# Kernel tuning notes

Hardware: AMD Instinct MI355X
Metric: run time of the kernel (lower is better)

The kernel has to match this reference:

```python
import jax, jax.numpy as jnp
import numpy as np

DIM = 2048
BATCH = 64


def setup_inputs() -> dict:
    key = jax.random.key(0)
    kx, kq, kk, kv = jax.random.split(key, 4)
    s = 1.0 / np.sqrt(DIM).astype(np.float32)  # keep q*k logits O(1)
    x = jax.random.normal(kx, (BATCH, DIM), dtype=jnp.float32)
    Wq = jax.random.normal(kq, (DIM, DIM), dtype=jnp.float32) * s
    Wk = jax.random.normal(kk, (DIM, DIM), dtype=jnp.float32) * s
    Wv = jax.random.normal(kv, (DIM, DIM), dtype=jnp.float32) * s
    return {"x": x, "Wq": Wq, "Wk": Wk, "Wv": Wv}


def reference(x, Wq, Wk, Wv):
    # nn.Linear(dim, inner_dim, bias=False): y = x @ W.T, W: [inner_dim, dim]
    q = x @ Wq.T  # [b, N]  (head_dim = 1, so each token's q is a scalar)
    k = x @ Wk.T  # [b, N]
    v = x @ Wv.T  # [b, N]
    # dot[b,i,j] = q[b,i] * k[b,j]  (rank-1 outer product per batch)
    logits = q[:, :, None] * k[:, None, :]  # [b, N, N]
    attn = jax.nn.softmax(logits, axis=-1)
    out = jnp.einsum("bij,bj->bi", attn, v)  # [b, N]
    # dim == inner_dim -> scale is Identity
    return out
```

## Files before the change

### kernel.cpp

```cpp
#include <hip/hip_runtime.h>
#include <hip/hip_bf16.h>

#define DIM 2048
#define NB  64
#define KSL 4
#define JSL 2

typedef short bf16x8 __attribute__((ext_vector_type(8)));
typedef short s16x4  __attribute__((ext_vector_type(4)));
typedef float f32x4  __attribute__((ext_vector_type(4)));
typedef float f32x2  __attribute__((ext_vector_type(2)));

__device__ __forceinline__ unsigned short f32_to_bf16_rne(float f) {
  unsigned u = __builtin_bit_cast(unsigned, f);
  unsigned r = u + 0x7FFF + ((u >> 16) & 1);
  return (unsigned short)(r >> 16);
}

__global__ __launch_bounds__(256)
void prep(const float* __restrict__ x, unsigned short* __restrict__ xrh,
          unsigned short* __restrict__ xrl, float* __restrict__ qkv) {
  const int tg = blockIdx.x * 256 + threadIdx.x;
#pragma unroll
  for (int z = 0; z < 3; ++z)
    *(float4*)(qkv + ((size_t)z * 32768 + tg) * 4) = make_float4(0.f,0.f,0.f,0.f);

  const int b = tg >> 9;
  const int k = (tg & 511) * 4;
  float4 f = *(const float4*)(x + (size_t)b * DIM + k);
  const int mt = b >> 4, l15 = b & 15;
  const int ck = k >> 5, quad = (k >> 3) & 3, u = k & 7;
  const size_t off = (((size_t)(mt * 64 + ck) * 64) + quad * 16 + l15) * 8 + u;
  float vf[4] = {f.x, f.y, f.z, f.w};
  ushort4 h4, l4;
  unsigned short* hp = &h4.x;
  unsigned short* lp = &l4.x;
#pragma unroll
  for (int e = 0; e < 4; ++e) {
    unsigned short h = f32_to_bf16_rne(vf[e]);
    float hf = __builtin_bit_cast(float, ((unsigned)h) << 16);
    hp[e] = h;
    lp[e] = f32_to_bf16_rne(vf[e] - hf);
  }
  *(ushort4*)(xrh + off) = h4;
  *(ushort4*)(xrl + off) = l4;
}

#define WSTR 260

__device__ __forceinline__ void conv_store_w(short (*wh)[WSTR], short (*wl)[WSTR],
                                             const float4* wreg, int wave, int lane) {
#pragma unroll
  for (int p = 0; p < 8; ++p) {
    const int r = p * 4 + wave;
    float wf[4] = {wreg[p].x, wreg[p].y, wreg[p].z, wreg[p].w};
    s16x4 h4, l4;
#pragma unroll
    for (int e = 0; e < 4; ++e) {
      unsigned uu = __builtin_bit_cast(unsigned, wf[e]);
      h4[e] = (short)(uu >> 16);
      float hf = __builtin_bit_cast(float, uu & 0xFFFF0000u);
      float res = wf[e] - hf;
      l4[e] = (short)(__builtin_bit_cast(unsigned, res) >> 16);
    }
    *(s16x4*)&wh[r][lane * 4] = h4;
    *(s16x4*)&wl[r][lane * 4] = l4;
  }
}

__global__ __launch_bounds__(256)
void qkv_mfma(const unsigned short* __restrict__ xrh,
              const unsigned short* __restrict__ xrl,
              const float* __restrict__ Wq, const float* __restrict__ Wk,
              const float* __restrict__ Wv, float* __restrict__ qkv) {
  const int mat = blockIdx.z;
  const float* __restrict__ W = (mat == 0) ? Wq : ((mat == 1) ? Wk : Wv);
  const int t = threadIdx.x;
  const int wave = t >> 6, lane = t & 63;
  const int l15 = lane & 15, quad = lane >> 4;
  const int j0 = blockIdx.x * 32;
  const int kb0 = blockIdx.y * 512;

  __shared__ __align__(16) short wh[32][WSTR];
  __shared__ __align__(16) short wl[32][WSTR];

  const int jh = wave & 1;
  const int mh = wave >> 1;
  const int frow = jh * 16 + l15;
  f32x4 acc[2] = {{0.f,0.f,0.f,0.f},{0.f,0.f,0.f,0.f}};

  float4 wa[8], wb[8];
#pragma unroll
  for (int p = 0; p < 8; ++p)
    wa[p] = *(const float4*)(W + (size_t)(j0 + p * 4 + wave) * DIM + kb0 + lane * 4);

#pragma unroll
  for (int c = 0; c < 2; ++c) {
    if (c == 0) conv_store_w(wh, wl, wa, wave, lane);
    else        conv_store_w(wh, wl, wb, wave, lane);
    if (c == 0) {
#pragma unroll
      for (int p = 0; p < 8; ++p)
        wb[p] = *(const float4*)(W + (size_t)(j0 + p * 4 + wave) * DIM +
                                 kb0 + 256 + lane * 4);
    }
    __syncthreads();

    const int ckb = blockIdx.y * 16 + c * 8;
#pragma unroll
    for (int kk = 0; kk < 8; ++kk) {
      bf16x8 whf, wlf;
      *(s16x4*)&whf       = *(const s16x4*)&wh[frow][kk * 32 + quad * 8];
      *(((s16x4*)&whf)+1) = *(const s16x4*)&wh[frow][kk * 32 + quad * 8 + 4];
      *(s16x4*)&wlf       = *(const s16x4*)&wl[frow][kk * 32 + quad * 8];
      *(((s16x4*)&wlf)+1) = *(const s16x4*)&wl[frow][kk * 32 + quad * 8 + 4];
      const int ck = ckb + kk;
#pragma unroll
      for (int u = 0; u < 2; ++u) {
        const int mt = mh * 2 + u;
        const size_t xo = (((size_t)(mt * 64 + ck)) * 64 + lane) * 8;
        bf16x8 ah = *(const bf16x8*)(xrh + xo);
        bf16x8 al = *(const bf16x8*)(xrl + xo);
        acc[u] = __builtin_amdgcn_mfma_f32_16x16x32_bf16(ah, whf, acc[u], 0, 0, 0);
        acc[u] = __builtin_amdgcn_mfma_f32_16x16x32_bf16(al, whf, acc[u], 0, 0, 0);
        acc[u] = __builtin_amdgcn_mfma_f32_16x16x32_bf16(ah, wlf, acc[u], 0, 0, 0);
      }
    }
    if (c == 0) __syncthreads();
  }

  float* __restrict__ pb = qkv + (size_t)mat * NB * DIM + j0 + jh * 16 + l15;
#pragma unroll
  for (int u = 0; u < 2; ++u)
#pragma unroll
    for (int r = 0; r < 4; ++r) {
      const int b = (mh * 2 + u) * 16 + quad * 4 + r;
      atomicAdd(pb + (size_t)b * DIM, acc[u][r]);
    }
}

__global__ __launch_bounds__(256)
void attn(const float* __restrict__ qkv, f32x2* __restrict__ pnd) {
  const int b = blockIdx.z, js = blockIdx.y;
  const int i = blockIdx.x * 256 + threadIdx.x;
  const float qi = qkv[(size_t)b * DIM + i];
  const float c = qi * 1.4426950408889634f;
  const float* __restrict__ kp = qkv + (size_t)(NB + b) * DIM + js * (DIM / JSL);
  const float* __restrict__ vp = qkv + (size_t)(2 * NB + b) * DIM + js * (DIM / JSL);

  float num[4] = {0.f, 0.f, 0.f, 0.f};
  float den[4] = {0.f, 0.f, 0.f, 0.f};
#pragma unroll 2
  for (int j = 0; j < DIM / JSL; j += 8) {
    float kb[8], vb[8];
#pragma unroll
    for (int u = 0; u < 8; ++u) { kb[u] = kp[j + u]; vb[u] = vp[j + u]; }
#pragma unroll
    for (int u = 0; u < 8; ++u) {
      float e = __builtin_amdgcn_exp2f(c * kb[u]);
      den[u & 3] += e;
      num[u & 3] = fmaf(e, vb[u], num[u & 3]);
    }
  }
  f32x2 nd;
  nd.x = (num[0] + num[1]) + (num[2] + num[3]);
  nd.y = (den[0] + den[1]) + (den[2] + den[3]);
  pnd[((size_t)b * JSL + js) * DIM + i] = nd;
}

__global__ __launch_bounds__(256)
void attn_fin(const f32x2* __restrict__ pnd, float* __restrict__ out) {
  const int b = blockIdx.y;
  const int i = blockIdx.x * 256 + threadIdx.x;
  float n = 0.f, d = 0.f;
#pragma unroll
  for (int s = 0; s < JSL; ++s) {
    f32x2 p = pnd[((size_t)b * JSL + s) * DIM + i];
    n += p.x; d += p.y;
  }
  out[(size_t)b * DIM + i] = n / d;
}

extern "C" void kernel_launch(void* const* d_in, const int* in_sizes, int n_in,
                              void* d_out, int out_size, void* d_ws, size_t ws_size,
                              hipStream_t stream) {
  const float* x  = (const float*)d_in[0];
  const float* Wq = (const float*)d_in[1];
  const float* Wk = (const float*)d_in[2];
  const float* Wv = (const float*)d_in[3];
  float* out = (float*)d_out;

  char* w = (char*)d_ws;
  unsigned short* xrh = (unsigned short*)w;
  unsigned short* xrl = (unsigned short*)(w + (512 << 10));
  float* qkv = (float*)(w + (1 << 20));
  f32x2* pnd = (f32x2*)(w + (4 << 20));

  hipLaunchKernelGGL(prep, dim3(128), dim3(256), 0, stream, x, xrh, xrl, qkv);
  hipLaunchKernelGGL(qkv_mfma, dim3(64, KSL, 3), dim3(256), 0, stream,
                     xrh, xrl, Wq, Wk, Wv, qkv);
  hipLaunchKernelGGL(attn, dim3(8, JSL, NB), dim3(256), 0, stream, qkv, pnd);
  hipLaunchKernelGGL(attn_fin, dim3(8, NB), dim3(256), 0, stream, pnd, out);
}
```

Baseline: 145.1 us.

## Compute attention weighted sums with bf16 MFMA and drop the split-J finalize kernel

The attention stage now uses one MFMA kernel. Each wave handles 16 query rows, computes exp2 scores for 32 keys per step, packs them to bf16, and multiplies them against a B fragment whose column 0 holds V and column 1 holds ones. This yields the numerator and denominator together on the matrix cores, and a shuffle-based divide writes the output directly. It removes the scalar FMA accumulation, the partial-sum buffer and the separate finalize launch, but rounds the exp weights and V to bf16, which loses precision. The MFMA also wastes 14 of its 16 output columns.

```diff
diff --git a/kernel.cpp b/kernel.cpp
--- a/kernel.cpp
+++ b/kernel.cpp
@@ -4,17 +4,24 @@
 #define DIM 2048
 #define NB  64
 #define KSL 4
-#define JSL 2
 
 typedef short bf16x8 __attribute__((ext_vector_type(8)));
 typedef short s16x4  __attribute__((ext_vector_type(4)));
 typedef float f32x4  __attribute__((ext_vector_type(4)));
-typedef float f32x2  __attribute__((ext_vector_type(2)));
 
 __device__ __forceinline__ unsigned short f32_to_bf16_rne(float f) {
   unsigned u = __builtin_bit_cast(unsigned, f);
   unsigned r = u + 0x7FFF + ((u >> 16) & 1);
   return (unsigned short)(r >> 16);
+}
+
+__device__ __forceinline__ s16x4 pk_bf16_4(float a, float b, float c, float d) {
+  s16x4 r;
+  r[0] = (short)f32_to_bf16_rne(a);
+  r[1] = (short)f32_to_bf16_rne(b);
+  r[2] = (short)f32_to_bf16_rne(c);
+  r[3] = (short)f32_to_bf16_rne(d);
+  return r;
 }
 
 __global__ __launch_bounds__(256)
@@ -140,45 +147,58 @@
 }
 
 __global__ __launch_bounds__(256)
-void attn(const float* __restrict__ qkv, f32x2* __restrict__ pnd) {
-  const int b = blockIdx.z, js = blockIdx.y;
-  const int i = blockIdx.x * 256 + threadIdx.x;
-  const float qi = qkv[(size_t)b * DIM + i];
-  const float c = qi * 1.4426950408889634f;
-  const float* __restrict__ kp = qkv + (size_t)(NB + b) * DIM + js * (DIM / JSL);
-  const float* __restrict__ vp = qkv + (size_t)(2 * NB + b) * DIM + js * (DIM / JSL);
-
-  float num[4] = {0.f, 0.f, 0.f, 0.f};
-  float den[4] = {0.f, 0.f, 0.f, 0.f};
+void attn_mfma(const float* __restrict__ qkv, float* __restrict__ out) {
+  const int b = blockIdx.y;
+  const int wave = threadIdx.x >> 6, lane = threadIdx.x & 63;
+  const int l15 = lane & 15, quad = lane >> 4;
+  const int it = blockIdx.x * 4 + wave;
+  const float* __restrict__ kp = qkv + (size_t)(NB + b) * DIM;
+  const float* __restrict__ vp = qkv + (size_t)(2 * NB + b) * DIM;
+  const float c = qkv[(size_t)b * DIM + it * 16 + l15] * 1.4426950408889634f;
+
+  const short one_bf = (short)0x3F80;
+  s16x4 cfrag = {0, 0, 0, 0};
+  if (l15 == 1) { cfrag[0] = one_bf; cfrag[1] = one_bf; cfrag[2] = one_bf; cfrag[3] = one_bf; }
+  const bool isv = (l15 == 0);
+
+  f32x4 acc = {0.f, 0.f, 0.f, 0.f};
 #pragma unroll 2
-  for (int j = 0; j < DIM / JSL; j += 8) {
-    float kb[8], vb[8];
-#pragma unroll
-    for (int u = 0; u < 8; ++u) { kb[u] = kp[j + u]; vb[u] = vp[j + u]; }
-#pragma unroll
-    for (int u = 0; u < 8; ++u) {
-      float e = __builtin_amdgcn_exp2f(c * kb[u]);
-      den[u & 3] += e;
-      num[u & 3] = fmaf(e, vb[u], num[u & 3]);
-    }
-  }
-  f32x2 nd;
-  nd.x = (num[0] + num[1]) + (num[2] + num[3]);
-  nd.y = (den[0] + den[1]) + (den[2] + den[3]);
-  pnd[((size_t)b * JSL + js) * DIM + i] = nd;
-}
-
-__global__ __launch_bounds__(256)
-void attn_fin(const f32x2* __restrict__ pnd, float* __restrict__ out) {
-  const int b = blockIdx.y;
-  const int i = blockIdx.x * 256 + threadIdx.x;
-  float n = 0.f, d = 0.f;
-#pragma unroll
-  for (int s = 0; s < JSL; ++s) {
-    f32x2 p = pnd[((size_t)b * JSL + s) * DIM + i];
-    n += p.x; d += p.y;
-  }
-  out[(size_t)b * DIM + i] = n / d;
+  for (int j0 = 0; j0 < DIM; j0 += 32) {
+    const int jb = j0 + quad * 8;
+    float4 k0 = *(const float4*)(kp + jb);
+    float4 k1 = *(const float4*)(kp + jb + 4);
+    float4 v0 = *(const float4*)(vp + jb);
+    float4 v1 = *(const float4*)(vp + jb + 4);
+    float e0 = __builtin_amdgcn_exp2f(c * k0.x);
+    float e1 = __builtin_amdgcn_exp2f(c * k0.y);
+    float e2 = __builtin_amdgcn_exp2f(c * k0.z);
+    float e3 = __builtin_amdgcn_exp2f(c * k0.w);
+    float e4 = __builtin_amdgcn_exp2f(c * k1.x);
+    float e5 = __builtin_amdgcn_exp2f(c * k1.y);
+    float e6 = __builtin_amdgcn_exp2f(c * k1.z);
+    float e7 = __builtin_amdgcn_exp2f(c * k1.w);
+    bf16x8 efrag;
+    *(s16x4*)&efrag         = pk_bf16_4(e0, e1, e2, e3);
+    *(((s16x4*)&efrag) + 1) = pk_bf16_4(e4, e5, e6, e7);
+    s16x4 vlo = pk_bf16_4(v0.x, v0.y, v0.z, v0.w);
+    s16x4 vhi = pk_bf16_4(v1.x, v1.y, v1.z, v1.w);
+    bf16x8 bfrag;
+    *(s16x4*)&bfrag         = isv ? vlo : cfrag;
+    *(((s16x4*)&bfrag) + 1) = isv ? vhi : cfrag;
+    acc = __builtin_amdgcn_mfma_f32_16x16x32_bf16(efrag, bfrag, acc, 0, 0, 0);
+  }
+
+  float d0 = __shfl_xor(acc[0], 1);
+  float d1 = __shfl_xor(acc[1], 1);
+  float d2 = __shfl_xor(acc[2], 1);
+  float d3 = __shfl_xor(acc[3], 1);
+  if (l15 == 0) {
+    float* __restrict__ ob = out + (size_t)b * DIM + it * 16 + quad * 4;
+    ob[0] = acc[0] / d0;
+    ob[1] = acc[1] / d1;
+    ob[2] = acc[2] / d2;
+    ob[3] = acc[3] / d3;
+  }
 }
 
 extern "C" void kernel_launch(void* const* d_in, const int* in_sizes, int n_in,
@@ -194,11 +214,9 @@
   unsigned short* xrh = (unsigned short*)w;
   unsigned short* xrl = (unsigned short*)(w + (512 << 10));
   float* qkv = (float*)(w + (1 << 20));
-  f32x2* pnd = (f32x2*)(w + (4 << 20));
 
   hipLaunchKernelGGL(prep, dim3(128), dim3(256), 0, stream, x, xrh, xrl, qkv);
   hipLaunchKernelGGL(qkv_mfma, dim3(64, KSL, 3), dim3(256), 0, stream,
                      xrh, xrl, Wq, Wk, Wv, qkv);
-  hipLaunchKernelGGL(attn, dim3(8, JSL, NB), dim3(256), 0, stream, qkv, pnd);
-  hipLaunchKernelGGL(attn_fin, dim3(8, NB), dim3(256), 0, stream, pnd, out);
-}
+  hipLaunchKernelGGL(attn_mfma, dim3(32, NB), dim3(256), 0, stream, qkv, out);
+}
```

Measured after the change: 181.5 us. 25.1% more time.
